# Kernel optimization log

Hardware: AMD Instinct MI355X
Metric: run time of the kernel (lower is better)

## Reference

```python
import jax, jax.numpy as jnp
import numpy as np
from jax import lax

# Geometry constants (match init_kwargs): cone-beam, flat panel detector.
W = H = D = 256          # image_size (w, h, d), voxels
NCOL, NROW = 384, 64     # num_det (col, row)
PIX = 1.0                # pix_size (mm)
DET_U, DET_V = 1.2, 1.2  # det_size (col, row) (mm)
ISO, SDD = 500.0, 1000.0 # iso_source, source_detector (mm)
NVIEW = 16
NSAMP = 256              # ray samples across the volume diagonal
RAY_LEN = float(np.sqrt(3.0)) * W * PIX
DT = RAY_LEN / NSAMP     # sampling step along each ray (mm)


def _trilinear(vol, x, y, z):
    """Trilinear sampling of vol [D,H,W] at voxel-index coords (x,y,z); zero outside."""
    x0 = jnp.floor(x); y0 = jnp.floor(y); z0 = jnp.floor(z)
    fx, fy, fz = x - x0, y - y0, z - z0
    x0 = x0.astype(jnp.int32); y0 = y0.astype(jnp.int32); z0 = z0.astype(jnp.int32)

    def fetch(zi, yi, xi):
        inb = (xi >= 0) & (xi < W) & (yi >= 0) & (yi < H) & (zi >= 0) & (zi < D)
        v = vol[jnp.clip(zi, 0, D - 1), jnp.clip(yi, 0, H - 1), jnp.clip(xi, 0, W - 1)]
        return jnp.where(inb, v, jnp.zeros((), vol.dtype))

    out = jnp.zeros(x.shape, vol.dtype)
    for dz, wz in ((0, 1.0 - fz), (1, fz)):
        for dy, wy in ((0, 1.0 - fy), (1, fy)):
            for dx, wx in ((0, 1.0 - fx), (1, fx)):
                out = out + wz * wy * wx * fetch(z0 + dz, y0 + dy, x0 + dx)
    return out


def _project(vol, angles):
    """Cone-beam flat-detector line integrals. vol [D,H,W] -> sino [V,NROW,NCOL]."""
    dt = vol.dtype
    u = ((jnp.arange(NCOL, dtype=dt) - NCOL / 2 + 0.5) * DET_U)  # detector col coords
    v = ((jnp.arange(NROW, dtype=dt) - NROW / 2 + 0.5) * DET_V)  # detector row coords
    t = ISO - RAY_LEN / 2 + (jnp.arange(NSAMP, dtype=dt) + 0.5) * DT  # sample dists

    def one_view(beta):
        cb, sb = jnp.cos(beta), jnp.sin(beta)
        zero = jnp.zeros_like(beta)
        src = jnp.stack([ISO * cb, ISO * sb, zero])          # source position
        ctr = jnp.stack([-(SDD - ISO) * cb, -(SDD - ISO) * sb, zero])  # detector center
        uax = jnp.stack([-sb, cb, zero])                      # detector col axis
        vax = jnp.array([0.0, 0.0, 1.0], dtype=dt)            # detector row axis (z)
        det = ctr + v[:, None, None] * vax + u[None, :, None] * uax   # [NROW,NCOL,3]
        d = det - src
        d = d / jnp.linalg.norm(d, axis=-1, keepdims=True)
        pts = src + t[:, None, None, None] * d[None]          # [S,NROW,NCOL,3]
        vx = pts[..., 0] / PIX + (W - 1) / 2
        vy = pts[..., 1] / PIX + (H - 1) / 2
        vz = pts[..., 2] / PIX + (D - 1) / 2
        return _trilinear(vol, vx, vy, vz).sum(0) * DT        # [NROW,NCOL]

    return lax.map(one_view, angles)                          # [V,NROW,NCOL]


def setup_inputs() -> dict:
    key = jax.random.key(0)
    image = jax.random.normal(key, (1, 1, D, H, W), dtype=jnp.float32)
    angles = jnp.linspace(0.0, 2.0 * np.pi, NVIEW, endpoint=False, dtype=jnp.float32)
    return {"image": image, "angles": angles}


def reference(image, angles):
    # image: [B,C,D,H,W] -> sino: [B,C,V,NROW,NCOL]
    return jax.vmap(jax.vmap(lambda vol: _project(vol, angles)))(image)
```

## Files before the change

### kernel.cpp

```cpp
#include <hip/hip_runtime.h>
#include <hip/hip_fp16.h>
#include <math.h>

namespace {
constexpr int NCOL = 384, NROW = 64, NVIEW = 16, NSAMP = 256;
constexpr float DET_U = 1.2f, DET_V = 1.2f;
constexpr float ISO = 500.0f, SDD = 1000.0f;
constexpr double SQRT3 = 1.7320508075688772;
constexpr float DT = (float)SQRT3;
constexpr float T0 = (float)(500.0 - SQRT3 * 256.0 * 0.5);
constexpr size_t VOL_N = 256u * 256u * 256u;
}

__device__ __forceinline__ void axis_interval(float p0, float d, float LO, float HI,
                                              float& tlo, float& thi) {
    if (fabsf(d) < 1e-7f) {
        if (p0 < LO || p0 > HI) { tlo = 1e30f; thi = -1e30f; }
        else                    { tlo = -1e30f; thi = 1e30f; }
    } else {
        const float r = 1.0f / d;
        const float t1 = (LO - p0) * r, t2 = (HI - p0) * r;
        tlo = fminf(t1, t2); thi = fmaxf(t1, t2);
    }
}

__device__ __forceinline__ float sample_shell(const float* __restrict__ vol,
                                              float vx, float vy, float vz) {
    if (!(vx > -1.0f && vx < 256.0f && vy > -1.0f && vy < 256.0f &&
          vz > -1.0f && vz < 256.0f))
        return 0.0f;
    const float fx0 = floorf(vx), fy0 = floorf(vy), fz0 = floorf(vz);
    const int x0 = (int)fx0, y0 = (int)fy0, z0 = (int)fz0;
    const float fx = vx - fx0, fy = vy - fy0, fz = vz - fz0;
    float sum = 0.0f;
    #pragma unroll
    for (int dzz = 0; dzz < 2; ++dzz) {
        const float wz = dzz ? fz : 1.0f - fz;
        const int zi = z0 + dzz;
        #pragma unroll
        for (int dyy = 0; dyy < 2; ++dyy) {
            const float wy = dyy ? fy : 1.0f - fy;
            const int yi = y0 + dyy;
            #pragma unroll
            for (int dxx = 0; dxx < 2; ++dxx) {
                const float wx = dxx ? fx : 1.0f - fx;
                const int xi = x0 + dxx;
                if ((unsigned)xi < 256u && (unsigned)yi < 256u && (unsigned)zi < 256u)
                    sum += wz * wy * wx * vol[(zi << 16) | (yi << 8) | xi];
            }
        }
    }
    return sum;
}

struct Spans { int g0, s0, s1, g1; float dx, dy, dz, bx, by, bz; float cb, sb; };

__device__ __forceinline__ Spans ray_setup(const float* __restrict__ angles, int tid) {
    Spans sp;
    const int col = tid % NCOL;
    const int rv  = tid / NCOL;
    const int row = rv % NROW;
    const int view = rv / NROW;

    const float beta = angles[view];
    const float cb = cosf(beta), sb = sinf(beta);
    sp.cb = cb; sp.sb = sb;
    const float u = (col - NCOL * 0.5f + 0.5f) * DET_U;
    const float v = (row - NROW * 0.5f + 0.5f) * DET_V;

    const float sx = ISO * cb, sy = ISO * sb;
    const float detx = -(SDD - ISO) * cb - u * sb;
    const float dety = -(SDD - ISO) * sb + u * cb;
    const float detz = v;

    float dx = detx - sx, dy = dety - sy, dz = detz;
    const float inv = 1.0f / sqrtf(dx * dx + dy * dy + dz * dz);
    dx *= inv; dy *= inv; dz *= inv;
    sp.dx = dx; sp.dy = dy; sp.dz = dz;
    sp.bx = sx + 127.5f; sp.by = sy + 127.5f; sp.bz = 127.5f;

    float xl, xh, yl, yh, zl, zh;
    axis_interval(sp.bx, dx, 0.01f, 254.99f, xl, xh);
    axis_interval(sp.by, dy, 0.01f, 254.99f, yl, yh);
    axis_interval(sp.bz, dz, 0.01f, 254.99f, zl, zh);
    const float tin  = fmaxf(xl, fmaxf(yl, zl));
    const float tout = fminf(xh, fminf(yh, zh));

    axis_interval(sp.bx, dx, -1.05f, 256.05f, xl, xh);
    axis_interval(sp.by, dy, -1.05f, 256.05f, yl, yh);
    axis_interval(sp.bz, dz, -1.05f, 256.05f, zl, zh);
    const float glo = fmaxf(xl, fmaxf(yl, zl));
    const float ghi = fminf(xh, fminf(yh, zh));

    const float invdt = 1.0f / DT;
    float g0f = floorf((glo - T0) * invdt - 0.5f);
    float g1f = ceilf((ghi - T0) * invdt - 0.5f) + 1.0f;
    float s0f = ceilf((tin - T0) * invdt - 0.5f + 0.01f);
    float s1f = floorf((tout - T0) * invdt - 0.5f - 0.01f) + 1.0f;
    int g0 = (int)fminf(fmaxf(g0f, 0.0f), 256.0f);
    int g1 = (int)fminf(fmaxf(g1f, 0.0f), 256.0f);
    int s0 = (int)fminf(fmaxf(s0f, 0.0f), 256.0f);
    int s1 = (int)fminf(fmaxf(s1f, 0.0f), 256.0f);
    s0 = max(s0, g0); s1 = min(s1, g1);
    if (s1 < s0) { s0 = g0; s1 = g0; }
    sp.g0 = g0; sp.s0 = s0; sp.s1 = s1; sp.g1 = g1;
    return sp;
}

__global__ __launch_bounds__(256) void packBoth_kernel(const float* __restrict__ vol,
                                                       __half2* __restrict__ P,
                                                       __half2* __restrict__ PT) {
    __shared__ __half2 tile[32][33];
    const int z = blockIdx.z;
    const int z1 = (z < 255) ? z + 1 : 255;
    const int x0 = blockIdx.x * 32, y0 = blockIdx.y * 32;
    const int tx = threadIdx.x, ty = threadIdx.y;
    const float* s0 = vol + (z  << 16);
    const float* s1 = vol + (z1 << 16);
    __half2* Pp = P + (z << 16);
    #pragma unroll
    for (int i = 0; i < 32; i += 8) {
        const int idx = ((y0 + ty + i) << 8) | (x0 + tx);
        const __half2 h = __floats2half2_rn(s0[idx], s1[idx]);
        Pp[idx] = h;
        tile[ty + i][tx] = h;
    }
    __syncthreads();
    __half2* Tp = PT + (z << 16);
    #pragma unroll
    for (int i = 0; i < 32; i += 8)
        Tp[((x0 + ty + i) << 8) | (y0 + tx)] = tile[tx][ty + i];
}

__device__ __forceinline__ float zlerp(__half2 q, float fc) {
    const float lo = __low2float(q), hi = __high2float(q);
    return fmaf(fc, hi - lo, lo);
}

struct Smp { float fa, fb, fc; __half2 q00, q01, q10, q11; };

__global__ __launch_bounds__(256) void projector3d_zp_kernel(
    const float* __restrict__ vol,
    const __half2* __restrict__ P,
    const __half2* __restrict__ PT,
    const float* __restrict__ angles,
    float* __restrict__ out)
{
    const int tid = blockIdx.x * 256 + threadIdx.x;

    const Spans sp = ray_setup(angles, tid);
    const float dx = sp.dx, dy = sp.dy, dz = sp.dz;
    const float bx = sp.bx, by = sp.by, bz = sp.bz;

    const bool useT = fabsf(sp.cb) > fabsf(sp.sb);
    const __half2* __restrict__ Pm = useT ? PT : P;
    const float da = useT ? dy : dx, db = useT ? dx : dy;
    const float ba = useT ? by : bx, bb = useT ? bx : by;

    float acc = 0.0f;

    for (int s = sp.g0; s < sp.s0; ++s) {
        const float t = T0 + (s + 0.5f) * DT;
        acc += sample_shell(vol, fmaf(t, dx, bx), fmaf(t, dy, by), fmaf(t, dz, bz));
    }

    auto LOADS = [&](Smp& S, int si) {
        const float t = T0 + (si + 0.5f) * DT;
        const float va = fmaf(t, da, ba), vb = fmaf(t, db, bb), vc = fmaf(t, dz, bz);
        const float a0 = floorf(va), b0 = floorf(vb), c0 = floorf(vc);
        S.fa = va - a0; S.fb = vb - b0; S.fc = vc - c0;
        const __half2* p = Pm + (((int)c0 << 16) | ((int)b0 << 8) | (int)a0);
        S.q00 = p[0]; S.q01 = p[1]; S.q10 = p[256]; S.q11 = p[257];
    };
    auto CONS = [&](const Smp& S) -> float {
        const float v00 = zlerp(S.q00, S.fc), v01 = zlerp(S.q01, S.fc);
        const float v10 = zlerp(S.q10, S.fc), v11 = zlerp(S.q11, S.fc);
        const float c0 = fmaf(S.fa, v01 - v00, v00);
        const float c1 = fmaf(S.fa, v11 - v10, v10);
        return fmaf(S.fb, c1 - c0, c0);
    };

    {
        int s = sp.s0;
        const int s1 = sp.s1;
        if (s < s1) {
            Smp A, B;
            LOADS(A, s);
            if (s + 1 < s1) {
                LOADS(B, s + 1);
                s += 2;
                for (; s + 1 < s1; s += 2) {
                    acc += CONS(A); LOADS(A, s);
                    acc += CONS(B); LOADS(B, s + 1);
                }
                if (s < s1) {
                    acc += CONS(A); LOADS(A, s);
                    acc += CONS(B);
                    acc += CONS(A);
                } else {
                    acc += CONS(A);
                    acc += CONS(B);
                }
            } else {
                acc += CONS(A);
            }
        }
    }

    for (int s2 = sp.s1; s2 < sp.g1; ++s2) {
        const float t = T0 + (s2 + 0.5f) * DT;
        acc += sample_shell(vol, fmaf(t, dx, bx), fmaf(t, dy, by), fmaf(t, dz, bz));
    }

    out[tid] = acc * DT;
}

__global__ __launch_bounds__(256) void transpose_kernel(const float* __restrict__ vol,
                                                        float* __restrict__ volT) {
    __shared__ float tile[32][33];
    const int z = blockIdx.z;
    const int x0 = blockIdx.x * 32, y0 = blockIdx.y * 32;
    const int tx = threadIdx.x, ty = threadIdx.y;
    const float* src = vol + (z << 16);
    float* dst = volT + (z << 16);
    #pragma unroll
    for (int i = 0; i < 32; i += 8)
        tile[ty + i][tx] = src[((y0 + ty + i) << 8) | (x0 + tx)];
    __syncthreads();
    #pragma unroll
    for (int i = 0; i < 32; i += 8)
        dst[((x0 + ty + i) << 8) | (y0 + tx)] = tile[tx][ty + i];
}

__global__ __launch_bounds__(256) void projector3d_dual_kernel(
    const float* __restrict__ vol, const float* __restrict__ volT,
    const float* __restrict__ angles, float* __restrict__ out)
{
    const int tid = blockIdx.x * 256 + threadIdx.x;
    const Spans sp = ray_setup(angles, tid);
    const float dx = sp.dx, dy = sp.dy, dz = sp.dz;
    const float bx = sp.bx, by = sp.by, bz = sp.bz;
    const bool useT = fabsf(sp.cb) > fabsf(sp.sb);
    const float* __restrict__ Pm = useT ? volT : vol;
    const float da = useT ? dy : dx, db = useT ? dx : dy;
    const float ba = useT ? by : bx, bb = useT ? bx : by;

    float acc = 0.0f;
    for (int s = sp.g0; s < sp.s0; ++s) {
        const float t = T0 + (s + 0.5f) * DT;
        acc += sample_shell(vol, fmaf(t, dx, bx), fmaf(t, dy, by), fmaf(t, dz, bz));
    }
    for (int s = sp.s0; s < sp.s1; ++s) {
        const float t = T0 + (s + 0.5f) * DT;
        const float va = fmaf(t, da, ba), vb = fmaf(t, db, bb), vc = fmaf(t, dz, bz);
        const float fa0 = floorf(va), fb0 = floorf(vb), fc0 = floorf(vc);
        const float fa = va - fa0, fb = vb - fb0, fc = vc - fc0;
        const float* p = Pm + (((int)fc0 << 16) | ((int)fb0 << 8) | (int)fa0);
        const float v000 = p[0],     v001 = p[1];
        const float v010 = p[256],   v011 = p[257];
        const float v100 = p[65536], v101 = p[65537];
        const float v110 = p[65792], v111 = p[65793];
        const float c00 = fmaf(fa, v001 - v000, v000);
        const float c01 = fmaf(fa, v011 - v010, v010);
        const float c10 = fmaf(fa, v101 - v100, v100);
        const float c11 = fmaf(fa, v111 - v110, v110);
        const float c0 = fmaf(fb, c01 - c00, c00);
        const float c1 = fmaf(fb, c11 - c10, c10);
        acc += fmaf(fc, c1 - c0, c0);
    }
    for (int s = sp.s1; s < sp.g1; ++s) {
        const float t = T0 + (s + 0.5f) * DT;
        acc += sample_shell(vol, fmaf(t, dx, bx), fmaf(t, dy, by), fmaf(t, dz, bz));
    }
    out[tid] = acc * DT;
}

__global__ __launch_bounds__(256) void projector3d_f32_kernel(
    const float* __restrict__ vol, const float* __restrict__ angles,
    float* __restrict__ out)
{
    const int tid = blockIdx.x * 256 + threadIdx.x;
    const Spans sp = ray_setup(angles, tid);
    const float dx = sp.dx, dy = sp.dy, dz = sp.dz;
    const float bx = sp.bx, by = sp.by, bz = sp.bz;
    float acc = 0.0f;
    for (int s = sp.g0; s < sp.s0; ++s) {
        const float t = T0 + (s + 0.5f) * DT;
        acc += sample_shell(vol, fmaf(t, dx, bx), fmaf(t, dy, by), fmaf(t, dz, bz));
    }
    #pragma unroll 4
    for (int s = sp.s0; s < sp.s1; ++s) {
        const float t = T0 + (s + 0.5f) * DT;
        const float vx = fmaf(t, dx, bx), vy = fmaf(t, dy, by), vz = fmaf(t, dz, bz);
        const float fx0 = floorf(vx), fy0 = floorf(vy), fz0 = floorf(vz);
        const int x0 = (int)fx0, y0 = (int)fy0, z0 = (int)fz0;
        const float fx = vx - fx0, fy = vy - fy0, fz = vz - fz0;
        const float* p = vol + ((z0 << 16) | (y0 << 8) | x0);
        const float v000 = p[0],     v001 = p[1];
        const float v010 = p[256],   v011 = p[257];
        const float v100 = p[65536], v101 = p[65537];
        const float v110 = p[65792], v111 = p[65793];
        const float c00 = fmaf(fx, v001 - v000, v000);
        const float c01 = fmaf(fx, v011 - v010, v010);
        const float c10 = fmaf(fx, v101 - v100, v100);
        const float c11 = fmaf(fx, v111 - v110, v110);
        const float c0 = fmaf(fy, c01 - c00, c00);
        const float c1 = fmaf(fy, c11 - c10, c10);
        acc += fmaf(fz, c1 - c0, c0);
    }
    for (int s = sp.s1; s < sp.g1; ++s) {
        const float t = T0 + (s + 0.5f) * DT;
        acc += sample_shell(vol, fmaf(t, dx, bx), fmaf(t, dy, by), fmaf(t, dz, bz));
    }
    out[tid] = acc * DT;
}

extern "C" void kernel_launch(void* const* d_in, const int* in_sizes, int n_in,
                              void* d_out, int out_size, void* d_ws, size_t ws_size,
                              hipStream_t stream) {
    const float* vol    = (const float*)d_in[0];
    const float* angles = (const float*)d_in[1];
    float* out = (float*)d_out;

    const int grid = (NVIEW * NROW * NCOL) / 256;
    if (ws_size >= 2u * VOL_N * sizeof(__half2)) {
        __half2* P  = (__half2*)d_ws;
        __half2* PT = P + VOL_N;
        dim3 tgrid(8, 8, 256), tblk(32, 8);
        packBoth_kernel<<<tgrid, tblk, 0, stream>>>(vol, P, PT);
        projector3d_zp_kernel<<<grid, 256, 0, stream>>>(vol, P, PT, angles, out);
    } else if (ws_size >= VOL_N * sizeof(float)) {
        float* volT = (float*)d_ws;
        dim3 tgrid(8, 8, 256), tblk(32, 8);
        transpose_kernel<<<tgrid, tblk, 0, stream>>>(vol, volT);
        projector3d_dual_kernel<<<grid, 256, 0, stream>>>(vol, volT, angles, out);
    } else {
        projector3d_f32_kernel<<<grid, 256, 0, stream>>>(vol, angles, out);
    }
}
```

Measured before the change: 255.0 us.

## Pack x-neighbor half2 pairs into uint2 to halve per-sample gather loads

Adds a packing kernel that stores, for each voxel, its z-pair and its x+1 neighbor's z-pair together as a uint2, in both normal and transposed layouts. The projector then needs two 8-byte loads per sample instead of four 4-byte loads, cutting gather instruction count and cache-line touches. In exchange the workspace doubles to 256 MB and the pack kernel writes twice as much data, and the float32 transpose fallback path is removed.

```diff
diff --git a/kernel.cpp b/kernel.cpp
--- a/kernel.cpp
+++ b/kernel.cpp
@@ -107,6 +107,129 @@
     return sp;
 }
 
+__device__ __forceinline__ float zlerp_u(unsigned u, float fc) {
+    __half2 q; *reinterpret_cast<unsigned*>(&q) = u;
+    const float lo = __low2float(q), hi = __high2float(q);
+    return fmaf(fc, hi - lo, lo);
+}
+
+__global__ __launch_bounds__(256) void packAP_kernel(const float* __restrict__ vol,
+                                                     uint2* __restrict__ APd,
+                                                     uint2* __restrict__ APt) {
+    __shared__ __half2 lds[33][34];
+    const int z = blockIdx.z, z1 = (z < 255) ? z + 1 : 255;
+    const int x0 = blockIdx.x * 32, y0 = blockIdx.y * 32;
+    const int tx = threadIdx.x, ty = threadIdx.y;
+    const int tid = ty * 32 + tx;
+    const float* s0 = vol + (z  << 16);
+    const float* s1 = vol + (z1 << 16);
+    for (int idx = tid; idx < 33 * 33; idx += 256) {
+        const int yy = idx / 33, xx = idx - yy * 33;
+        const int gy = min(y0 + yy, 255), gx = min(x0 + xx, 255);
+        const int g = (gy << 8) | gx;
+        lds[yy][xx] = __floats2half2_rn(s0[g], s1[g]);
+    }
+    __syncthreads();
+    uint2* Dp = APd + (z << 16);
+    #pragma unroll
+    for (int i = 0; i < 32; i += 8) {
+        const int yy = ty + i;
+        __half2 e0 = lds[yy][tx], e1 = lds[yy][tx + 1];
+        uint2 q;
+        q.x = *reinterpret_cast<unsigned*>(&e0);
+        q.y = *reinterpret_cast<unsigned*>(&e1);
+        Dp[((y0 + yy) << 8) | (x0 + tx)] = q;
+    }
+    uint2* Tp = APt + (z << 16);
+    #pragma unroll
+    for (int i = 0; i < 32; i += 8) {
+        const int r = ty + i;
+        __half2 e0 = lds[tx][r], e1 = lds[tx + 1][r];
+        uint2 q;
+        q.x = *reinterpret_cast<unsigned*>(&e0);
+        q.y = *reinterpret_cast<unsigned*>(&e1);
+        Tp[((x0 + r) << 8) | (y0 + tx)] = q;
+    }
+}
+
+struct SmpA { float fa, fb, fc; uint2 r0, r1; };
+
+__global__ __launch_bounds__(256) void projector3d_ap_kernel(
+    const float* __restrict__ vol,
+    const uint2* __restrict__ APd,
+    const uint2* __restrict__ APt,
+    const float* __restrict__ angles,
+    float* __restrict__ out)
+{
+    const int tid = blockIdx.x * 256 + threadIdx.x;
+
+    const Spans sp = ray_setup(angles, tid);
+    const float dx = sp.dx, dy = sp.dy, dz = sp.dz;
+    const float bx = sp.bx, by = sp.by, bz = sp.bz;
+
+    const bool useT = fabsf(sp.cb) > fabsf(sp.sb);
+    const uint2* __restrict__ Pm = useT ? APt : APd;
+    const float da = useT ? dy : dx, db = useT ? dx : dy;
+    const float ba = useT ? by : bx, bb = useT ? bx : by;
+
+    float acc = 0.0f;
+
+    for (int s = sp.g0; s < sp.s0; ++s) {
+        const float t = T0 + (s + 0.5f) * DT;
+        acc += sample_shell(vol, fmaf(t, dx, bx), fmaf(t, dy, by), fmaf(t, dz, bz));
+    }
+
+    auto LOADS = [&](SmpA& S, int si) {
+        const float t = T0 + (si + 0.5f) * DT;
+        const float va = fmaf(t, da, ba), vb = fmaf(t, db, bb), vc = fmaf(t, dz, bz);
+        const float a0 = floorf(va), b0 = floorf(vb), c0 = floorf(vc);
+        S.fa = va - a0; S.fb = vb - b0; S.fc = vc - c0;
+        const uint2* p = Pm + (((int)c0 << 16) | ((int)b0 << 8) | (int)a0);
+        S.r0 = p[0]; S.r1 = p[256];
+    };
+    auto CONS = [&](const SmpA& S) -> float {
+        const float v00 = zlerp_u(S.r0.x, S.fc), v01 = zlerp_u(S.r0.y, S.fc);
+        const float v10 = zlerp_u(S.r1.x, S.fc), v11 = zlerp_u(S.r1.y, S.fc);
+        const float c0 = fmaf(S.fa, v01 - v00, v00);
+        const float c1 = fmaf(S.fa, v11 - v10, v10);
+        return fmaf(S.fb, c1 - c0, c0);
+    };
+
+    {
+        int s = sp.s0;
+        const int s1 = sp.s1;
+        if (s < s1) {
+            SmpA A, B;
+            LOADS(A, s);
+            if (s + 1 < s1) {
+                LOADS(B, s + 1);
+                s += 2;
+                for (; s + 1 < s1; s += 2) {
+                    acc += CONS(A); LOADS(A, s);
+                    acc += CONS(B); LOADS(B, s + 1);
+                }
+                if (s < s1) {
+                    acc += CONS(A); LOADS(A, s);
+                    acc += CONS(B);
+                    acc += CONS(A);
+                } else {
+                    acc += CONS(A);
+                    acc += CONS(B);
+                }
+            } else {
+                acc += CONS(A);
+            }
+        }
+    }
+
+    for (int s2 = sp.s1; s2 < sp.g1; ++s2) {
+        const float t = T0 + (s2 + 0.5f) * DT;
+        acc += sample_shell(vol, fmaf(t, dx, bx), fmaf(t, dy, by), fmaf(t, dz, bz));
+    }
+
+    out[tid] = acc * DT;
+}
+
 __global__ __launch_bounds__(256) void packBoth_kernel(const float* __restrict__ vol,
                                                        __half2* __restrict__ P,
                                                        __half2* __restrict__ PT) {
@@ -147,23 +270,19 @@
     float* __restrict__ out)
 {
     const int tid = blockIdx.x * 256 + threadIdx.x;
-
     const Spans sp = ray_setup(angles, tid);
     const float dx = sp.dx, dy = sp.dy, dz = sp.dz;
     const float bx = sp.bx, by = sp.by, bz = sp.bz;
-
     const bool useT = fabsf(sp.cb) > fabsf(sp.sb);
     const __half2* __restrict__ Pm = useT ? PT : P;
     const float da = useT ? dy : dx, db = useT ? dx : dy;
     const float ba = useT ? by : bx, bb = useT ? bx : by;
 
     float acc = 0.0f;
-
     for (int s = sp.g0; s < sp.s0; ++s) {
         const float t = T0 + (s + 0.5f) * DT;
         acc += sample_shell(vol, fmaf(t, dx, bx), fmaf(t, dy, by), fmaf(t, dz, bz));
     }
-
     auto LOADS = [&](Smp& S, int si) {
         const float t = T0 + (si + 0.5f) * DT;
         const float va = fmaf(t, da, ba), vb = fmaf(t, db, bb), vc = fmaf(t, dz, bz);
@@ -179,7 +298,6 @@
         const float c1 = fmaf(S.fa, v11 - v10, v10);
         return fmaf(S.fb, c1 - c0, c0);
     };
-
     {
         int s = sp.s0;
         const int s1 = sp.s1;
@@ -206,70 +324,8 @@
             }
         }
     }
-
     for (int s2 = sp.s1; s2 < sp.g1; ++s2) {
         const float t = T0 + (s2 + 0.5f) * DT;
-        acc += sample_shell(vol, fmaf(t, dx, bx), fmaf(t, dy, by), fmaf(t, dz, bz));
-    }
-
-    out[tid] = acc * DT;
-}
-
-__global__ __launch_bounds__(256) void transpose_kernel(const float* __restrict__ vol,
-                                                        float* __restrict__ volT) {
-    __shared__ float tile[32][33];
-    const int z = blockIdx.z;
-    const int x0 = blockIdx.x * 32, y0 = blockIdx.y * 32;
-    const int tx = threadIdx.x, ty = threadIdx.y;
-    const float* src = vol + (z << 16);
-    float* dst = volT + (z << 16);
-    #pragma unroll
-    for (int i = 0; i < 32; i += 8)
-        tile[ty + i][tx] = src[((y0 + ty + i) << 8) | (x0 + tx)];
-    __syncthreads();
-    #pragma unroll
-    for (int i = 0; i < 32; i += 8)
-        dst[((x0 + ty + i) << 8) | (y0 + tx)] = tile[tx][ty + i];
-}
-
-__global__ __launch_bounds__(256) void projector3d_dual_kernel(
-    const float* __restrict__ vol, const float* __restrict__ volT,
-    const float* __restrict__ angles, float* __restrict__ out)
-{
-    const int tid = blockIdx.x * 256 + threadIdx.x;
-    const Spans sp = ray_setup(angles, tid);
-    const float dx = sp.dx, dy = sp.dy, dz = sp.dz;
-    const float bx = sp.bx, by = sp.by, bz = sp.bz;
-    const bool useT = fabsf(sp.cb) > fabsf(sp.sb);
-    const float* __restrict__ Pm = useT ? volT : vol;
-    const float da = useT ? dy : dx, db = useT ? dx : dy;
-    const float ba = useT ? by : bx, bb = useT ? bx : by;
-
-    float acc = 0.0f;
-    for (int s = sp.g0; s < sp.s0; ++s) {
-        const float t = T0 + (s + 0.5f) * DT;
-        acc += sample_shell(vol, fmaf(t, dx, bx), fmaf(t, dy, by), fmaf(t, dz, bz));
-    }
-    for (int s = sp.s0; s < sp.s1; ++s) {
-        const float t = T0 + (s + 0.5f) * DT;
-        const float va = fmaf(t, da, ba), vb = fmaf(t, db, bb), vc = fmaf(t, dz, bz);
-        const float fa0 = floorf(va), fb0 = floorf(vb), fc0 = floorf(vc);
-        const float fa = va - fa0, fb = vb - fb0, fc = vc - fc0;
-        const float* p = Pm + (((int)fc0 << 16) | ((int)fb0 << 8) | (int)fa0);
-        const float v000 = p[0],     v001 = p[1];
-        const float v010 = p[256],   v011 = p[257];
-        const float v100 = p[65536], v101 = p[65537];
-        const float v110 = p[65792], v111 = p[65793];
-        const float c00 = fmaf(fa, v001 - v000, v000);
-        const float c01 = fmaf(fa, v011 - v010, v010);
-        const float c10 = fmaf(fa, v101 - v100, v100);
-        const float c11 = fmaf(fa, v111 - v110, v110);
-        const float c0 = fmaf(fb, c01 - c00, c00);
-        const float c1 = fmaf(fb, c11 - c10, c10);
-        acc += fmaf(fc, c1 - c0, c0);
-    }
-    for (int s = sp.s1; s < sp.g1; ++s) {
-        const float t = T0 + (s + 0.5f) * DT;
         acc += sample_shell(vol, fmaf(t, dx, bx), fmaf(t, dy, by), fmaf(t, dz, bz));
     }
     out[tid] = acc * DT;
@@ -323,17 +379,17 @@
     float* out = (float*)d_out;
 
     const int grid = (NVIEW * NROW * NCOL) / 256;
-    if (ws_size >= 2u * VOL_N * sizeof(__half2)) {
+    dim3 tgrid(8, 8, 256), tblk(32, 8);
+    if (ws_size >= 2u * VOL_N * sizeof(uint2)) {
+        uint2* APd = (uint2*)d_ws;
+        uint2* APt = APd + VOL_N;
+        packAP_kernel<<<tgrid, tblk, 0, stream>>>(vol, APd, APt);
+        projector3d_ap_kernel<<<grid, 256, 0, stream>>>(vol, APd, APt, angles, out);
+    } else if (ws_size >= 2u * VOL_N * sizeof(__half2)) {
         __half2* P  = (__half2*)d_ws;
         __half2* PT = P + VOL_N;
-        dim3 tgrid(8, 8, 256), tblk(32, 8);
         packBoth_kernel<<<tgrid, tblk, 0, stream>>>(vol, P, PT);
         projector3d_zp_kernel<<<grid, 256, 0, stream>>>(vol, P, PT, angles, out);
-    } else if (ws_size >= VOL_N * sizeof(float)) {
-        float* volT = (float*)d_ws;
-        dim3 tgrid(8, 8, 256), tblk(32, 8);
-        transpose_kernel<<<tgrid, tblk, 0, stream>>>(vol, volT);
-        projector3d_dual_kernel<<<grid, 256, 0, stream>>>(vol, volT, angles, out);
     } else {
         projector3d_f32_kernel<<<grid, 256, 0, stream>>>(vol, angles, out);
     }
```

Measured after the change: 270.1 us. +5.9%, slower.
